# Kernel tuning notes

Measured on AMD Instinct MI355X. Metric: run time of the kernel, lower is better.

The kernel has to match this reference:

```python
import jax, jax.numpy as jnp
import numpy as np

NUM_EMBEDDINGS = 16384
EMBEDDING_DIM = 256
B, C, H, W = 8, 256, 32, 32


def _l2_normalize(x, axis=-1, eps=1e-12):
    # matches torch.nn.functional.normalize(p=2): x / max(||x||, eps)
    n = jnp.sqrt(jnp.sum(x * x, axis=axis, keepdims=True))
    return x / jnp.maximum(n, eps)


def setup_inputs() -> dict:
    key = jax.random.key(0)
    k1, k2 = jax.random.split(key)
    z = jax.random.normal(k1, (B, C, H, W), dtype=jnp.float32)
    embedding_weight = jax.random.normal(k2, (NUM_EMBEDDINGS, EMBEDDING_DIM), dtype=jnp.float32)
    return {"z": z, "embedding_weight": embedding_weight}


def reference(z, embedding_weight):
    batch_size, channels, height, width = z.shape
    # [B,C,H,W] -> [B,H,W,C] -> [N, D]
    z_flat = jnp.transpose(z, (0, 2, 3, 1)).reshape(-1, EMBEDDING_DIM)
    z_flat = _l2_normalize(z_flat)                 # l2_norm=True
    emb = _l2_normalize(embedding_weight)
    # squared distances: ||z||^2 + ||e||^2 - 2 z e^T  -> [N, K]
    d = (jnp.sum(z_flat * z_flat, axis=1, keepdims=True)
         + jnp.sum(emb * emb, axis=1)
         - 2.0 * jnp.matmul(z_flat, emb.T))
    indices = jnp.argmin(d, axis=1)                # [N]
    z_q = emb[indices].reshape(batch_size, height, width, EMBEDDING_DIM)
    z_q = jnp.transpose(z_q, (0, 3, 1, 2))         # [B,C,H,W]
    indices = indices.reshape(batch_size, height, width)
    return z_q, indices
```

## Files before the change

### kernel.cpp

```cpp
#include <hip/hip_runtime.h>

#define NUM_E   16384
#define DIM     256
#define NROWS   8192
#define HW      1024
#define BM      128
#define BN      256
#define NCB     (NUM_E / BN)
#define GATE    2.5e-3f
#define TAUC    2.5e-3f
#define EHID    2.5e-3
#define MAXC    16

typedef __bf16 bf16x8 __attribute__((ext_vector_type(8)));
typedef float  f32x16 __attribute__((ext_vector_type(16)));

__device__ __forceinline__ unsigned short f2bf(float x) {
    unsigned u = __float_as_uint(x);
    unsigned r = (u + 0x7fffu + ((u >> 16) & 1u)) >> 16;
    return (unsigned short)r;
}
__device__ __forceinline__ int imax(int a, int b) { return a > b ? a : b; }
__device__ __forceinline__ int imin(int a, int b) { return a < b ? a : b; }
__device__ __forceinline__ bf16x8 ld16(const unsigned short* p) {
    return *(const bf16x8*)p;
}
__device__ __forceinline__ size_t faddr(int row, int kk) {
    return ((size_t)((row >> 5) * 16 + (kk >> 4))) * 512
         + ((row & 31) + ((kk >> 3) & 1) * 32) * 8 + (kk & 7);
}
__device__ __forceinline__ unsigned long long packqv(double qv, int k) {
    return (((unsigned long long)__double_as_longlong(qv + 2.0)) & ~0x3FFFull)
         | (unsigned long long)(0x3FFF - k);
}

__global__ void k_pre(const float* __restrict__ z, const float* __restrict__ emb,
                      float* __restrict__ zpart, float* __restrict__ inv_e,
                      double* __restrict__ se2, unsigned short* __restrict__ Eh,
                      int* __restrict__ cnt, int* __restrict__ cnt2) {
    int bid = blockIdx.x;
    if (bid < NUM_E / 4) {
        if (bid == 0 && threadIdx.x == 0) { *cnt = 0; *cnt2 = 0; }
        int wv = threadIdx.x >> 6, lane = threadIdx.x & 63;
        int k = bid * 4 + wv;
        float4 v = *(const float4*)(emb + (size_t)k * DIM + lane * 4);
        double sq = (double)v.x*v.x + (double)v.y*v.y + (double)v.z*v.z + (double)v.w*v.w;
        for (int off = 32; off > 0; off >>= 1) sq += __shfl_down(sq, off);
        double tot = fmax(__shfl(sq, 0), 1e-24);
        if (lane == 0) { se2[k] = tot; inv_e[k] = 1.0f / fmaxf((float)sqrt(tot), 1e-12f); }
        float s = 1.0f / fmaxf((float)sqrt(tot), 1e-12f);
        ushort4 h;
        h.x = f2bf(v.x * s); h.y = f2bf(v.y * s); h.z = f2bf(v.z * s); h.w = f2bf(v.w * s);
        *(ushort4*)(Eh + faddr(k, lane * 4)) = h;
    } else {
        int ib = bid - NUM_E / 4;
        int n = (ib & 31) * 256 + threadIdx.x;
        int cb = ib >> 5;
        int b = n >> 10, hw = n & 1023;
        const float* p = z + (size_t)(b * DIM + cb * 16) * HW + hw;
        float s = 0.f;
        #pragma unroll
        for (int c = 0; c < 16; c++) { float v = p[c * HW]; s += v * v; }
        zpart[cb * NROWS + n] = s;
    }
}

__global__ void k_prep_z(const float* __restrict__ z, const float* __restrict__ zpart,
                         unsigned short* __restrict__ Zh) {
    __shared__ float T[64 * 68];
    __shared__ __align__(16) float Tinv[64];
    int t = threadIdx.x;
    int n0 = blockIdx.x * 64, c0 = blockIdx.y * 64;
    int b = n0 >> 10, hw0 = n0 & 1023;
    if (t < 64) {
        float s = 0.f;
        #pragma unroll
        for (int cb = 0; cb < 16; cb++) s += zpart[cb * NROWS + n0 + t];
        Tinv[t] = 1.0f / fmaxf(sqrtf(s), 1e-12f);
    }
    __syncthreads();
    #pragma unroll
    for (int i = 0; i < 4; i++) {
        int f = t + 256 * i;
        int cc = f >> 4, n4 = (f & 15) * 4;
        float4 v  = *(const float4*)(z + (size_t)(b * DIM + c0 + cc) * HW + hw0 + n4);
        float4 iv = *(const float4*)&Tinv[n4];
        v.x *= iv.x; v.y *= iv.y; v.z *= iv.z; v.w *= iv.w;
        *(float4*)&T[cc * 68 + n4] = v;
    }
    __syncthreads();
    #pragma unroll
    for (int i = 0; i < 4; i++) {
        int f = t + 256 * i;
        int nn = f >> 4, c4 = (f & 15) * 4;
        ushort4 h;
        h.x = f2bf(T[(c4+0)*68 + nn]);
        h.y = f2bf(T[(c4+1)*68 + nn]);
        h.z = f2bf(T[(c4+2)*68 + nn]);
        h.w = f2bf(T[(c4+3)*68 + nn]);
        *(ushort4*)(Zh + faddr(n0 + nn, c0 + c4)) = h;
    }
}

__launch_bounds__(256, 2)
__global__ void k_score(const unsigned short* __restrict__ Zh,
                        const unsigned short* __restrict__ Eh, int2* __restrict__ part) {
    __shared__ __align__(16) int kv[8448];
    const int t = threadIdx.x, l = t & 63, w = t >> 6;
    const int wm = w >> 1, wn = w & 1;
    int bid = blockIdx.x;
    int rr2 = (bid & 7) * 512 + (bid >> 3);
    int st = rr2 >> 6, wi = rr2 & 63;
    const int m0 = ((st >> 3) * 8 + (wi >> 3)) * BM;
    const int nb = ((st & 7) * 8 + (wi & 7)) * BN;
    const int l31 = l & 31, lh = l >> 5;

    const unsigned short* pa0 = Zh + ((size_t)((m0 >> 5) + wm * 2 + 0) * 16) * 512 + l * 8;
    const unsigned short* pa1 = Zh + ((size_t)((m0 >> 5) + wm * 2 + 1) * 16) * 512 + l * 8;
    const unsigned short* pb0 = Eh + ((size_t)((nb >> 5) + wn * 4 + 0) * 16) * 512 + l * 8;
    const unsigned short* pb1 = Eh + ((size_t)((nb >> 5) + wn * 4 + 1) * 16) * 512 + l * 8;
    const unsigned short* pb2 = Eh + ((size_t)((nb >> 5) + wn * 4 + 2) * 16) * 512 + l * 8;
    const unsigned short* pb3 = Eh + ((size_t)((nb >> 5) + wn * 4 + 3) * 16) * 512 + l * 8;

    f32x16 acc[2][4];
    #pragma unroll
    for (int i = 0; i < 2; i++)
        #pragma unroll
        for (int j = 0; j < 4; j++) acc[i][j] = (f32x16)2.0f;

    bf16x8 fr[3][6];
#define LDS3(s, OFF) \
    fr[s][0] = ld16(pa0 + (OFF)); fr[s][1] = ld16(pa1 + (OFF)); \
    fr[s][2] = ld16(pb0 + (OFF)); fr[s][3] = ld16(pb1 + (OFF)); \
    fr[s][4] = ld16(pb2 + (OFF)); fr[s][5] = ld16(pb3 + (OFF));

    LDS3(0, 0); LDS3(1, 512);
    #pragma unroll
    for (int ks = 0; ks < 16; ks++) {
        const int s = ks % 3;
        if (ks + 2 < 16) { const int s2 = (ks + 2) % 3; LDS3(s2, (ks + 2) * 512); }
        __builtin_amdgcn_s_setprio(1);
        #pragma unroll
        for (int i = 0; i < 2; i++)
            #pragma unroll
            for (int j = 0; j < 4; j++)
                acc[i][j] = __builtin_amdgcn_mfma_f32_32x32x16_bf16(fr[s][i], fr[s][2 + j], acc[i][j], 0, 0, 0);
        __builtin_amdgcn_s_setprio(0);
    }
#undef LDS3

    const int colbase = wn * 128 + l31;
    int KA1 = 0, KA2 = 0, KB1 = 0, KB2 = 0;
    const int rl = t >> 2, q = t & 3;
    #pragma unroll
    for (int i = 0; i < 2; i++) {
        #pragma unroll
        for (int reg = 0; reg < 16; reg++) {
            int k0 = (__float_as_int(acc[i][0][reg]) & 0xFFFFFF00) | colbase;
            int k1 = (__float_as_int(acc[i][1][reg]) & 0xFFFFFF00) | (colbase + 32);
            int k2 = (__float_as_int(acc[i][2][reg]) & 0xFFFFFF00) | (colbase + 64);
            int k3 = (__float_as_int(acc[i][3][reg]) & 0xFFFFFF00) | (colbase + 96);
            int a = imax(k0, k1), b = imin(k0, k1);
            int c = imax(k2, k3), d = imin(k2, k3);
            int K1 = imax(a, c);
            int K2 = imax(imin(a, c), imax(b, d));
            int rr = wm * 32 + (reg & 3) + 8 * (reg >> 2) + 4 * lh;
            int slot = wn * 32 + l31;
            *(int2*)&kv[(rr * 66 + slot) * 2] = make_int2(K1, K2);
        }
        __syncthreads();
        int S1 = 0, S2 = 0;
        const int2* pr = (const int2*)&kv[(rl * 66 + q * 16) * 2];
        #pragma unroll
        for (int u = 0; u < 16; u++) {
            int2 e = pr[u];
            S2 = imax(imax(S2, e.y), imin(S1, e.x));
            S1 = imax(S1, e.x);
        }
        __syncthreads();
        #pragma unroll
        for (int d2 = 1; d2 <= 2; d2 <<= 1) {
            int o1 = __shfl_down(S1, d2), o2 = __shfl_down(S2, d2);
            S2 = imax(imax(S2, o2), imin(S1, o1));
            S1 = imax(S1, o1);
        }
        if (i == 0) { KA1 = S1; KA2 = S2; } else { KB1 = S1; KB2 = S2; }
    }
    if ((t & 3) == 0) {
        int rowA = (rl >> 5) * 64 + (rl & 31);
        int rowB = rowA + 32;
        int seg = nb / BN;
        part[(size_t)seg * NROWS + m0 + rowA] = make_int2(KA1, KA2);
        part[(size_t)seg * NROWS + m0 + rowB] = make_int2(KB1, KB2);
    }
}

__global__ void k_final(const int2* __restrict__ part, int* __restrict__ idx_ws,
                        float* __restrict__ out_idx, int* __restrict__ flags,
                        int* __restrict__ cnt, int* __restrict__ cand,
                        int* __restrict__ ccnt, float* __restrict__ v2q,
                        int* __restrict__ bm) {
    __shared__ int rK1[8][33], rK2[8][33], rS[8][33];
    __shared__ int bK1[32], bK2[32];
    __shared__ int lcc[32];
    __shared__ int lcand[32][MAXC];
    __shared__ int sv2[8][33];
    const int nl = threadIdx.x & 31, sc = threadIdx.x >> 5;
    const int n = blockIdx.x * 32 + nl;
    if (threadIdx.x < 32) lcc[threadIdx.x] = 0;
    int K1 = 0, K2 = 0, S1 = 0;
    for (int s = sc * 8; s < sc * 8 + 8; s++) {
        int2 e = part[(size_t)s * NROWS + n];
        S1 = (e.x > K1) ? s : S1;
        int nK2 = imax(imin(K1, e.x), imax(K2, e.y));
        K1 = imax(K1, e.x);
        K2 = nK2;
    }
    rK1[sc][nl] = K1; rK2[sc][nl] = K2; rS[sc][nl] = S1;
    __syncthreads();
    if (threadIdx.x < 32) {
        int W1 = 0, W2 = 0, WS = 0;
        #pragma unroll
        for (int s2 = 0; s2 < 8; s2++) {
            int e1 = rK1[s2][threadIdx.x], e2 = rK2[s2][threadIdx.x];
            WS = (e1 > W1) ? rS[s2][threadIdx.x] : WS;
            int nW2 = imax(imin(W1, e1), imax(W2, e2));
            W1 = imax(W1, e1);
            W2 = nW2;
        }
        int nn = blockIdx.x * 32 + threadIdx.x;
        int J1 = WS * BN + (W1 & 0xFF);
        idx_ws[nn] = J1;
        out_idx[nn] = (float)J1;
        bK1[threadIdx.x] = W1;
        bK2[threadIdx.x] = W2;
        bm[nn] = 0;
    }
    __syncthreads();
    int kthr = __float_as_int(__int_as_float(bK1[nl] & 0xFFFFFF00) - TAUC);
    int lv2 = 0;
    for (int s = sc * 8; s < sc * 8 + 8; s++) {
        int2 e = part[(size_t)s * NROWS + n];
        if (e.x >= kthr) {
            int pos = atomicAdd(&lcc[nl], 2);
            if (pos < MAXC)     lcand[nl][pos]     = s * BN + (e.x & 0xFF);
            if (pos + 1 < MAXC) lcand[nl][pos + 1] = s * BN + (e.y & 0xFF);
            lv2 = imax(lv2, e.y);
        }
    }
    sv2[sc][nl] = lv2;
    __syncthreads();
    if (threadIdx.x < 32) {
        int nn = blockIdx.x * 32 + threadIdx.x;
        float v1 = __int_as_float(bK1[threadIdx.x] & 0xFFFFFF00) - 2.0f;
        float v2 = __int_as_float(bK2[threadIdx.x] & 0xFFFFFF00) - 2.0f;
        if (v1 - v2 < GATE) {
            int m = 0;
            #pragma unroll
            for (int s2 = 0; s2 < 8; s2++) m = imax(m, sv2[s2][threadIdx.x]);
            int p = atomicAdd(cnt, 1);
            flags[p] = nn;
            ccnt[nn] = lcc[threadIdx.x];
            v2q[nn] = __int_as_float(m & 0xFFFFFF00) - 2.0f;
            #pragma unroll
            for (int j = 0; j < MAXC; j++) cand[nn * MAXC + j] = lcand[threadIdx.x][j];
        }
    }
}

__launch_bounds__(256)
__global__ void k_rescan_cand(const int* __restrict__ flags, const int* __restrict__ cnt,
                              const int* __restrict__ cand, const int* __restrict__ ccnt,
                              const float* __restrict__ v2q,
                              const float* __restrict__ z, const float* __restrict__ emb,
                              const double* __restrict__ se2,
                              int* __restrict__ idx_ws, float* __restrict__ out_idx,
                              int* __restrict__ flags2, int* __restrict__ cnt2,
                              unsigned long long* __restrict__ slot, int* __restrict__ bm) {
    __shared__ double zs[DIM];
    __shared__ double wv[4];
    __shared__ int    wi[4];
    const int t = threadIdx.x, l = t & 63, w = t >> 6;
    const int F = *cnt;
    for (int f = blockIdx.x; f < F; f += gridDim.x) {
        int n = flags[f];
        int C = ccnt[n];
        int b = n >> 10, hw = n & 1023;
        __syncthreads();
        zs[t] = (double)z[(size_t)(b * DIM + t) * HW + hw];
        __syncthreads();
        double best = -2e18; int bi = 0x7fffffff;
        if (C <= MAXC) {
            double z0 = zs[l*4], z1 = zs[l*4+1], z2 = zs[l*4+2], z3 = zs[l*4+3];
            for (int cix = w; cix < C; cix += 4) {
                int k = cand[n * MAXC + cix];
                float4 ev = *(const float4*)(emb + (size_t)k * DIM + l * 4);
                double d = z0 * (double)ev.x + z1 * (double)ev.y
                         + z2 * (double)ev.z + z3 * (double)ev.w;
                #pragma unroll
                for (int o = 32; o > 0; o >>= 1) d += __shfl_down(d, o);
                if (l == 0) {
                    double qv = d / sqrt(se2[k]);
                    if (qv > best || (qv == best && k < bi)) { best = qv; bi = k; }
                }
            }
        }
        if (l == 0) { wv[w] = best; wi[w] = bi; }
        __syncthreads();
        if (t == 0) {
            bool esc = (C > MAXC);
            if (!esc) {
                double B = wv[0]; int BI = wi[0];
                #pragma unroll
                for (int x = 1; x < 4; x++)
                    if (wv[x] > B || (wv[x] == B && wi[x] < BI)) { B = wv[x]; BI = wi[x]; }
                if ((double)v2q[n] >= B - EHID) {
                    esc = true;
                } else {
                    idx_ws[n] = BI; out_idx[n] = (float)BI;
                }
            }
            if (esc) {
                slot[n] = 0ull;
                bm[n] = 1;
                int p = atomicAdd(cnt2, 1);
                flags2[p] = n;
            }
        }
        __syncthreads();
    }
}

__launch_bounds__(256)
__global__ void k_fullscan(const int* __restrict__ flags2, const int* __restrict__ cnt2,
                           const float* __restrict__ z, const float* __restrict__ emb,
                           const double* __restrict__ se2,
                           unsigned long long* __restrict__ slot) {
    __shared__ double zs[DIM];
    __shared__ double wv[4];
    __shared__ int    wi[4];
    const int t = threadIdx.x, l = t & 63, w = t >> 6;
    const int W = (*cnt2) * 64;
    for (int item = blockIdx.x; item < W; item += gridDim.x) {
        int f = item >> 6, split = item & 63;
        int n = flags2[f];
        int b = n >> 10, hw = n & 1023;
        __syncthreads();
        zs[t] = (double)z[(size_t)(b * DIM + t) * HW + hw];
        __syncthreads();
        double z0 = zs[l*4], z1 = zs[l*4+1], z2 = zs[l*4+2], z3 = zs[l*4+3];
        double best = -2e18; int bi = 0;
        int kbase = split * 256 + w * 64;
        for (int p = 0; p < 64; p++) {
            int k = kbase + p;
            float4 ev = *(const float4*)(emb + (size_t)k * DIM + l * 4);
            double d = z0 * (double)ev.x + z1 * (double)ev.y
                     + z2 * (double)ev.z + z3 * (double)ev.w;
            #pragma unroll
            for (int o = 32; o > 0; o >>= 1) d += __shfl_down(d, o);
            if (l == 0) {
                double qv = d / sqrt(se2[k]);
                if (qv > best || (qv == best && k < bi)) { best = qv; bi = k; }
            }
        }
        if (l == 0) { wv[w] = best; wi[w] = bi; }
        __syncthreads();
        if (t == 0) {
            double B = wv[0]; int BI = wi[0];
            #pragma unroll
            for (int x = 1; x < 4; x++)
                if (wv[x] > B || (wv[x] == B && wi[x] < BI)) { B = wv[x]; BI = wi[x]; }
            atomicMax(&slot[n], packqv(B, BI));
        }
        __syncthreads();
    }
}

__global__ void k_zq(const int* __restrict__ idx_ws, const float* __restrict__ emb,
                     const float* __restrict__ inv_e, float* __restrict__ zq,
                     const int* __restrict__ bm, const unsigned long long* __restrict__ slot,
                     float* __restrict__ out_idx) {
    int t = threadIdx.x;
    int n = blockIdx.x * 256 + t;
    int b = n >> 10, hw = n & 1023;
    int c0 = blockIdx.y * 32;
    int id = idx_ws[n];
    if (bm[n]) {
        id = 0x3FFF - (int)(slot[n] & 0x3FFFull);
        if (blockIdx.y == 0) out_idx[n] = (float)id;
    }
    float s = inv_e[id];
    const float* er = emb + (size_t)id * DIM;
    #pragma unroll
    for (int cc = 0; cc < 32; cc += 4) {
        float4 a = *(const float4*)(er + c0 + cc);
        zq[(size_t)(b * DIM + c0 + cc + 0) * HW + hw] = a.x * s;
        zq[(size_t)(b * DIM + c0 + cc + 1) * HW + hw] = a.y * s;
        zq[(size_t)(b * DIM + c0 + cc + 2) * HW + hw] = a.z * s;
        zq[(size_t)(b * DIM + c0 + cc + 3) * HW + hw] = a.w * s;
    }
}

extern "C" void kernel_launch(void* const* d_in, const int* in_sizes, int n_in,
                              void* d_out, int out_size, void* d_ws, size_t ws_size,
                              hipStream_t stream) {
    const float* z   = (const float*)d_in[0];
    const float* emb = (const float*)d_in[1];

    unsigned short* Zh = (unsigned short*)d_ws;
    unsigned short* Eh = Zh + (size_t)NROWS * DIM;
    float*  inv_e = (float*)(Eh + (size_t)NUM_E * DIM);
    float*  zpart = inv_e + NUM_E;
    int*    idx_ws = (int*)(zpart + 16 * NROWS);
    double* se2   = (double*)(idx_ws + NROWS);
    int*    flags = (int*)(se2 + NUM_E);
    int*    flags2 = flags + NROWS;
    int*    cand  = flags2 + NROWS;
    int*    ccnt  = cand + NROWS * MAXC;
    float*  v2q   = (float*)(ccnt + NROWS);
    int*    bm    = (int*)(v2q + NROWS);
    int*    cnt   = bm + NROWS;
    int*    cnt2  = cnt + 1;
    unsigned long long* slot = (unsigned long long*)zpart;

    float* zq      = (float*)d_out;
    float* out_idx = zq + (size_t)NROWS * DIM;
    int2* part = (int2*)zq;

    k_pre        <<<NUM_E / 4 + 512, 256, 0, stream>>>(z, emb, zpart, inv_e, se2, Eh, cnt, cnt2);
    k_prep_z     <<<dim3(NROWS / 64, DIM / 64), 256, 0, stream>>>(z, zpart, Zh);
    k_score      <<<(NROWS / BM) * NCB, 256, 0, stream>>>(Zh, Eh, part);
    k_final      <<<NROWS / 32, 256, 0, stream>>>(part, idx_ws, out_idx, flags, cnt,
                                                  cand, ccnt, v2q, bm);
    k_rescan_cand<<<1024, 256, 0, stream>>>(flags, cnt, cand, ccnt, v2q, z, emb, se2,
                                            idx_ws, out_idx, flags2, cnt2, slot, bm);
    k_fullscan   <<<2048, 256, 0, stream>>>(flags2, cnt2, z, emb, se2, slot);
    k_zq         <<<dim3(NROWS / 256, 8), 256, 0, stream>>>(idx_ws, emb, inv_e, zq,
                                                            bm, slot, out_idx);
}
```

Before: 169.8 us.

## Replace full-codebook fallback scan with window-pruned scan using per-chunk bf16 bounds

Result: no change. 169.5 us, median of 2 (-0.2%).

```diff
diff --git a/kernel.cpp b/kernel.cpp
--- a/kernel.cpp
+++ b/kernel.cpp
@@ -10,6 +10,7 @@
 #define GATE    2.5e-3f
 #define TAUC    2.5e-3f
 #define EHID    2.5e-3
+#define WINDOW  5e-3f
 #define MAXC    16
 
 typedef __bf16 bf16x8 __attribute__((ext_vector_type(8)));
@@ -28,10 +29,6 @@
 __device__ __forceinline__ size_t faddr(int row, int kk) {
     return ((size_t)((row >> 5) * 16 + (kk >> 4))) * 512
          + ((row & 31) + ((kk >> 3) & 1) * 32) * 8 + (kk & 7);
-}
-__device__ __forceinline__ unsigned long long packqv(double qv, int k) {
-    return (((unsigned long long)__double_as_longlong(qv + 2.0)) & ~0x3FFFull)
-         | (unsigned long long)(0x3FFF - k);
 }
 
 __global__ void k_pre(const float* __restrict__ z, const float* __restrict__ emb,
@@ -332,47 +329,63 @@
 }
 
 __launch_bounds__(256)
-__global__ void k_fullscan(const int* __restrict__ flags2, const int* __restrict__ cnt2,
-                           const float* __restrict__ z, const float* __restrict__ emb,
-                           const double* __restrict__ se2,
-                           unsigned long long* __restrict__ slot) {
-    __shared__ double zs[DIM];
-    __shared__ double wv[4];
-    __shared__ int    wi[4];
+__global__ void k_winscan(const int* __restrict__ flags2, const int* __restrict__ cnt2,
+                          const int2* __restrict__ part,
+                          const float* __restrict__ z, const float* __restrict__ emb,
+                          const float* __restrict__ inv_e,
+                          unsigned long long* __restrict__ slot) {
+    __shared__ __align__(16) float zs[DIM];
+    __shared__ int sK1[64], sK2[64];
+    __shared__ unsigned long long wbest[4];
     const int t = threadIdx.x, l = t & 63, w = t >> 6;
-    const int W = (*cnt2) * 64;
-    for (int item = blockIdx.x; item < W; item += gridDim.x) {
-        int f = item >> 6, split = item & 63;
+    const int F = *cnt2;
+    for (int f = blockIdx.x; f < F; f += gridDim.x) {
         int n = flags2[f];
         int b = n >> 10, hw = n & 1023;
         __syncthreads();
-        zs[t] = (double)z[(size_t)(b * DIM + t) * HW + hw];
-        __syncthreads();
-        double z0 = zs[l*4], z1 = zs[l*4+1], z2 = zs[l*4+2], z3 = zs[l*4+3];
-        double best = -2e18; int bi = 0;
-        int kbase = split * 256 + w * 64;
-        for (int p = 0; p < 64; p++) {
-            int k = kbase + p;
-            float4 ev = *(const float4*)(emb + (size_t)k * DIM + l * 4);
-            double d = z0 * (double)ev.x + z1 * (double)ev.y
-                     + z2 * (double)ev.z + z3 * (double)ev.w;
+        zs[t] = z[(size_t)(b * DIM + t) * HW + hw];
+        if (t < 64) {
+            int2 e = part[(size_t)t * NROWS + n];
+            sK1[t] = e.x; sK2[t] = e.y;
+        }
+        __syncthreads();
+        int K1 = 0;
+        #pragma unroll
+        for (int s = 0; s < 64; s++) K1 = imax(K1, sK1[s]);
+        float cosW1 = __int_as_float(K1 & 0xFFFFFF00) - 2.0f;
+        int thr = __float_as_int((cosW1 - WINDOW) + 2.0f) & 0xFFFFFF00;
+        unsigned long long best = 0ull;
+        for (int s = 0; s < 64; s++) {
+            if (imax(sK1[s], sK2[s]) < thr) continue;
+            int k = s * 256 + t;
+            const float4* er = (const float4*)(emb + (size_t)k * DIM);
+            float d0 = 0.f, d1 = 0.f, d2 = 0.f, d3 = 0.f;
             #pragma unroll
-            for (int o = 32; o > 0; o >>= 1) d += __shfl_down(d, o);
-            if (l == 0) {
-                double qv = d / sqrt(se2[k]);
-                if (qv > best || (qv == best && k < bi)) { best = qv; bi = k; }
+            for (int d4 = 0; d4 < 64; d4++) {
+                float4 ev = er[d4];
+                float4 zv = *(const float4*)&zs[d4 * 4];
+                d0 += zv.x * ev.x; d1 += zv.y * ev.y;
+                d2 += zv.z * ev.z; d3 += zv.w * ev.w;
             }
-        }
-        if (l == 0) { wv[w] = best; wi[w] = bi; }
+            float qv = ((d0 + d1) + (d2 + d3)) * inv_e[k];
+            unsigned long long key =
+                (((unsigned long long)__float_as_uint(qv + 32.0f)) << 14)
+                | (unsigned long long)(0x3FFF - k);
+            best = key > best ? key : best;
+        }
+        #pragma unroll
+        for (int o = 32; o > 0; o >>= 1) {
+            unsigned long long ob = __shfl_down(best, o);
+            best = ob > best ? ob : best;
+        }
+        if (l == 0) wbest[w] = best;
         __syncthreads();
         if (t == 0) {
-            double B = wv[0]; int BI = wi[0];
+            unsigned long long B = wbest[0];
             #pragma unroll
-            for (int x = 1; x < 4; x++)
-                if (wv[x] > B || (wv[x] == B && wi[x] < BI)) { B = wv[x]; BI = wi[x]; }
-            atomicMax(&slot[n], packqv(B, BI));
-        }
-        __syncthreads();
+            for (int x = 1; x < 4; x++) B = wbest[x] > B ? wbest[x] : B;
+            slot[n] = B;
+        }
     }
 }
 
@@ -434,7 +447,7 @@
                                                   cand, ccnt, v2q, bm);
     k_rescan_cand<<<1024, 256, 0, stream>>>(flags, cnt, cand, ccnt, v2q, z, emb, se2,
                                             idx_ws, out_idx, flags2, cnt2, slot, bm);
-    k_fullscan   <<<2048, 256, 0, stream>>>(flags2, cnt2, z, emb, se2, slot);
+    k_winscan    <<<1024, 256, 0, stream>>>(flags2, cnt2, part, z, emb, inv_e, slot);
     k_zq         <<<dim3(NROWS / 256, 8), 256, 0, stream>>>(idx_ws, emb, inv_e, zq,
                                                             bm, slot, out_idx);
 }
```
